# Kernel tuning notes

Hardware: AMD Instinct MI355X
Metric: run time of the kernel (lower is better)

Reference implementation:

```python
import jax, jax.numpy as jnp
import numpy as np

B, C, H, W = 2, 128, 96, 96
HEADS, DHEAD, WIN = 4, 32, 5
INNER = HEADS * DHEAD
PAD = WIN // 2


def setup_inputs() -> dict:
    key = jax.random.key(0)
    k1, k2, k3, k4, k5 = jax.random.split(key, 5)
    s = 1.0 / np.sqrt(C)
    return {
        "x": jax.random.normal(k1, (B, C, H, W), dtype=jnp.float32),
        "wq": jax.random.normal(k2, (INNER, C), dtype=jnp.float32) * s,
        "wk": jax.random.normal(k3, (INNER, C), dtype=jnp.float32) * s,
        "wv": jax.random.normal(k4, (INNER, C), dtype=jnp.float32) * s,
        "wproj": jax.random.normal(k5, (C, INNER), dtype=jnp.float32) * s,
    }


def _windows(t):
    # same neighborhood ordering as F.unfold (row-major over kernel offsets).
    tp = jnp.pad(t, ((0, 0), (0, 0), (0, 0), (PAD, PAD), (PAD, PAD)))
    wins = [tp[:, :, :, di:di + H, dj:dj + W]
            for di in range(WIN) for dj in range(WIN)]
    return jnp.stack(wins, axis=3)


def reference(x, wq, wk, wv, wproj):
    # 1x1 convs == per-pixel linear maps
    q = jnp.einsum('oc,bcxy->boxy', wq, x).reshape(B, HEADS, DHEAD, H, W)
    k = jnp.einsum('oc,bcxy->boxy', wk, x).reshape(B, HEADS, DHEAD, H, W)
    v = jnp.einsum('oc,bcxy->boxy', wv, x).reshape(B, HEADS, DHEAD, H, W)

    k_win = _windows(k)  # (B,h,d,25,H,W)
    v_win = _windows(v)

    scale = 1.0 / np.sqrt(DHEAD)
    attn = jnp.einsum('bhdxy,bhdkxy->bhkxy', q, k_win) * scale
    attn = jax.nn.softmax(attn, axis=2)  # softmax over the 25 window positions
    out = jnp.einsum('bhkxy,bhdkxy->bhdxy', attn, v_win)

    out = out.reshape(B, INNER, H, W)
    return jnp.einsum('co,boxy->bcxy', wproj, out)
```

## Files before the change

kernel.cpp:

```cpp
#include <hip/hip_runtime.h>
#include <hip/hip_fp16.h>

#define PP 9216

typedef _Float16 f16x8 __attribute__((ext_vector_type(8)));
typedef _Float16 f16x4 __attribute__((ext_vector_type(4)));
typedef _Float16 h2    __attribute__((ext_vector_type(2)));
typedef float    f32x4 __attribute__((ext_vector_type(4)));

#define LDS_BYTES 32768

__device__ __forceinline__ int swz128(int row, int hc) {
    return row * 128 + (((hc >> 3) ^ (row & 15)) << 3) + (hc & 7);
}
__device__ __forceinline__ int swz64(int row, int hc) {
    return row * 64 + (((hc >> 3) ^ (row & 7)) << 3) + (hc & 7);
}

__global__ __launch_bounds__(256) void prep_w(
    const float* __restrict__ wq, const float* __restrict__ wk,
    const float* __restrict__ wv, const float* __restrict__ wp,
    _Float16* __restrict__ wqkv16, _Float16* __restrict__ wp16)
{
    int e = (blockIdx.x * 256 + threadIdx.x) * 4;
    const float* src;
    _Float16* dst;
    if (e < 49152) {
        int o = e >> 7;
        src = (o < 128) ? (wq + (size_t)o * 128)
            : (o < 256) ? (wk + (size_t)(o - 128) * 128)
                        : (wv + (size_t)(o - 256) * 128);
        src += (e & 127);
        dst = wqkv16 + e;
    } else {
        int j = e - 49152;
        src = wp + j;
        dst = wp16 + j;
    }
    float4 v = *(const float4*)src;
    f16x4 h;
    h[0] = (_Float16)v.x; h[1] = (_Float16)v.y;
    h[2] = (_Float16)v.z; h[3] = (_Float16)v.w;
    *(f16x4*)dst = h;
}

__global__ __launch_bounds__(256, 5) void fused_attn(
    const float* __restrict__ x, const _Float16* __restrict__ wqkv,
    const _Float16* __restrict__ wp16, float* __restrict__ out)
{
    __shared__ __align__(16) char smem[LDS_BYTES];
    _Float16* sA = (_Float16*)smem;
    _Float16* sB = (_Float16*)(smem + 16384);

    const int t = threadIdx.x;
    const int w = t >> 6, lane = t & 63, lm = lane & 15, quad = lane >> 4;

    const int wgid = (blockIdx.x & 7) * 144 + (blockIdx.x >> 3);
    const int b = wgid / 576;
    const int rem = wgid - b * 576;
    const int x0 = (rem % 24) * 4, y0 = (rem / 24) * 4;

    const float* xb = x + (size_t)b * 128 * PP;
    float* ob = out + (size_t)b * 128 * PP;

    {
        const int pos = (t & 31) * 2;
        const int gy = y0 - 2 + (pos >> 3);
        const int gx = x0 - 2 + (pos & 7);
        const bool inb = ((unsigned)gy < 96u) && ((unsigned)gx < 96u);
        const float* src = xb + (size_t)(t >> 5) * PP + gy * 96 + gx;
        float2 vv[16];
        #pragma unroll
        for (int i = 0; i < 16; i++)
            vv[i] = inb ? *(const float2*)(src + (size_t)(i * 8) * PP)
                        : make_float2(0.f, 0.f);
        #pragma unroll
        for (int i = 0; i < 16; i++) {
            int c = i * 8 + (t >> 5);
            sA[swz128(pos,     c)] = (_Float16)vv[i].x;
            sA[swz128(pos + 1, c)] = (_Float16)vv[i].y;
        }
    }
    __syncthreads();

    h2 vpk[2][4][2];
    #pragma unroll
    for (int m = 0; m < 4; m++) {
        f16x8 A[4];
        #pragma unroll
        for (int kc = 0; kc < 4; kc++)
            A[kc] = *(const f16x8*)(sA + swz128(m * 16 + lm, kc * 32 + quad * 8));
        #pragma unroll
        for (int ni = 0; ni < 4; ni++) {
            const int wrow = (ni < 2) ? (128 + (w + 4 * ni) * 16 + lm)
                                      : (256 + (2 * w + (ni - 2)) * 16 + lm);
            const _Float16* wr = wqkv + (size_t)wrow * 128;
            f32x4 acc = {0.f, 0.f, 0.f, 0.f};
            #pragma unroll
            for (int kc = 0; kc < 4; kc++)
                acc = __builtin_amdgcn_mfma_f32_16x16x32_f16(
                    A[kc], *(const f16x8*)(wr + kc * 32 + quad * 8), acc, 0, 0, 0);
            if (ni < 2) {
                int n = w + 4 * ni;
                #pragma unroll
                for (int r = 0; r < 4; r++)
                    sB[swz128(m * 16 + quad * 4 + r, n * 16 + lm)] = (_Float16)acc[r];
            } else {
                h2 p0, p1;
                p0[0] = (_Float16)acc[0]; p0[1] = (_Float16)acc[1];
                p1[0] = (_Float16)acc[2]; p1[1] = (_Float16)acc[3];
                vpk[ni - 2][m][0] = p0;
                vpk[ni - 2][m][1] = p1;
            }
        }
    }

    f16x8 A3[4];
    {
        int hrow = ((lm >> 2) + 2) * 8 + (lm & 3) + 2;
        #pragma unroll
        for (int kc = 0; kc < 4; kc++)
            A3[kc] = *(const f16x8*)(sA + swz128(hrow, kc * 32 + quad * 8));
    }
    __syncthreads();

    _Float16* sQ = sA + 4608;
    #pragma unroll
    for (int nn = 0; nn < 2; nn++) {
        const _Float16* wr = wqkv + (size_t)((2 * w + nn) * 16 + lm) * 128;
        f32x4 acc = {0.f, 0.f, 0.f, 0.f};
        #pragma unroll
        for (int kc = 0; kc < 4; kc++)
            acc = __builtin_amdgcn_mfma_f32_16x16x32_f16(
                A3[kc], *(const f16x8*)(wr + kc * 32 + quad * 8), acc, 0, 0, 0);
        #pragma unroll
        for (int r = 0; r < 4; r++)
            sQ[swz128(quad * 4 + r, (2 * w + nn) * 16 + lm)] = (_Float16)acc[r];
    }

    f32x4 S[4];
    {
        f16x8 Aq = *(const f16x8*)(sQ + swz128(lm, w * 32 + quad * 8));
        #pragma unroll
        for (int n = 0; n < 4; n++) {
            f16x8 Bk = *(const f16x8*)(sB + swz128(n * 16 + lm, w * 32 + quad * 8));
            f32x4 z = {0.f, 0.f, 0.f, 0.f};
            S[n] = __builtin_amdgcn_mfma_f32_16x16x32_f16(Aq, Bk, z, 0, 0, 0);
        }
    }

    _Float16* sPh = sA + w * 1152;
    float inv4[4];
    {
        const float scale = 0.17677669529663689f;
        #pragma unroll
        for (int r = 0; r < 4; r++) {
            float e[4];
            float mx = -1e30f;
            #pragma unroll
            for (int n = 0; n < 4; n++) {
                int hy = n * 2 + (lm >> 3), hx = lm & 7;
                bool memb = (hy >= quad) && (hy < quad + 5) && (hx >= r) && (hx < r + 5);
                e[n] = memb ? S[n][r] * scale : -1e30f;
                mx = fmaxf(mx, e[n]);
            }
            mx = fmaxf(mx, __shfl_xor(mx, 1));
            mx = fmaxf(mx, __shfl_xor(mx, 2));
            mx = fmaxf(mx, __shfl_xor(mx, 4));
            mx = fmaxf(mx, __shfl_xor(mx, 8));
            float sum = 0.f;
            #pragma unroll
            for (int n = 0; n < 4; n++) {
                float ev = __expf(e[n] - mx);
                e[n] = ev;
                sum += ev;
            }
            sum += __shfl_xor(sum, 1);
            sum += __shfl_xor(sum, 2);
            sum += __shfl_xor(sum, 4);
            sum += __shfl_xor(sum, 8);
            inv4[r] = 1.f / sum;
            #pragma unroll
            for (int n = 0; n < 4; n++)
                sPh[(quad * 4 + r) * 72 + n * 16 + lm] = (_Float16)e[n];
        }
    }
    __syncthreads();

    _Float16* sVh = sB + w * 2048;
    #pragma unroll
    for (int nn = 0; nn < 2; nn++)
        #pragma unroll
        for (int m = 0; m < 4; m++)
            #pragma unroll
            for (int rp = 0; rp < 2; rp++)
                *(h2*)(sVh + swz64(nn * 16 + lm, m * 16 + quad * 4 + rp * 2))
                    = vpk[nn][m][rp];

    _Float16* sAo = sQ;
    {
        f16x8 Ap[2];
        #pragma unroll
        for (int kc = 0; kc < 2; kc++)
            Ap[kc] = *(const f16x8*)(sPh + lm * 72 + kc * 32 + quad * 8);
        #pragma unroll
        for (int nd = 0; nd < 2; nd++) {
            f32x4 acc = {0.f, 0.f, 0.f, 0.f};
            #pragma unroll
            for (int kc = 0; kc < 2; kc++) {
                f16x8 Bv = *(const f16x8*)(sVh + swz64(nd * 16 + lm, kc * 32 + quad * 8));
                acc = __builtin_amdgcn_mfma_f32_16x16x32_f16(Ap[kc], Bv, acc, 0, 0, 0);
            }
            #pragma unroll
            for (int r = 0; r < 4; r++)
                sAo[swz128(quad * 4 + r, w * 32 + nd * 16 + lm)] =
                    (_Float16)(acc[r] * inv4[r]);
        }
    }
    __syncthreads();

    {
        f16x8 Bf[4];
        #pragma unroll
        for (int kc = 0; kc < 4; kc++)
            Bf[kc] = *(const f16x8*)(sAo + swz128(lm, kc * 32 + quad * 8));
        int gp = (y0 + (lm >> 2)) * 96 + x0 + (lm & 3);
        #pragma unroll
        for (int mi = 0; mi < 2; mi++) {
            const _Float16* wr = wp16 + (size_t)((w * 2 + mi) * 16 + lm) * 128;
            f32x4 acc = {0.f, 0.f, 0.f, 0.f};
            #pragma unroll
            for (int kc = 0; kc < 4; kc++)
                acc = __builtin_amdgcn_mfma_f32_16x16x32_f16(
                    *(const f16x8*)(wr + kc * 32 + quad * 8), Bf[kc], acc, 0, 0, 0);
            int c0 = (w * 2 + mi) * 16 + quad * 4;
            #pragma unroll
            for (int r = 0; r < 4; r++)
                ob[(size_t)(c0 + r) * PP + gp] = acc[r];
        }
    }
}

extern "C" void kernel_launch(void* const* d_in, const int* in_sizes, int n_in,
                              void* d_out, int out_size, void* d_ws, size_t ws_size,
                              hipStream_t stream)
{
    const float* x  = (const float*)d_in[0];
    const float* wq = (const float*)d_in[1];
    const float* wk = (const float*)d_in[2];
    const float* wv = (const float*)d_in[3];
    const float* wp = (const float*)d_in[4];
    float* out = (float*)d_out;

    _Float16* wqkv16 = (_Float16*)d_ws;
    _Float16* wp16   = wqkv16 + 49152;

    prep_w<<<dim3(64), 256, 0, stream>>>(wq, wk, wv, wp, wqkv16, wp16);
    fused_attn<<<dim3(1152), 256, 0, stream>>>(x, wqkv16, wp16, out);
}
```

Before: 125.8 us.

## Split QKV projection into separate GEMM kernel to avoid halo recompute

Replaces the single fused kernel with two kernels. A standalone GEMM computes Q, K and V once per pixel into an fp16 pixel-major workspace. The attention kernel then gathers Q, K and V for each 4x4 tile plus its halo directly from global memory. This removes the roughly fourfold redundant K/V projection over 8x8 halo regions in the fused version, at the cost of an extra launch and a round trip of about 14 MB of fp16 intermediates through global memory and cache.

```diff
diff --git a/kernel.cpp b/kernel.cpp
--- a/kernel.cpp
+++ b/kernel.cpp
@@ -5,16 +5,20 @@
 
 typedef _Float16 f16x8 __attribute__((ext_vector_type(8)));
 typedef _Float16 f16x4 __attribute__((ext_vector_type(4)));
-typedef _Float16 h2    __attribute__((ext_vector_type(2)));
 typedef float    f32x4 __attribute__((ext_vector_type(4)));
-
-#define LDS_BYTES 32768
 
 __device__ __forceinline__ int swz128(int row, int hc) {
     return row * 128 + (((hc >> 3) ^ (row & 15)) << 3) + (hc & 7);
 }
 __device__ __forceinline__ int swz64(int row, int hc) {
     return row * 64 + (((hc >> 3) ^ (row & 7)) << 3) + (hc & 7);
+}
+
+__device__ __forceinline__ f16x8 zero8() {
+    f16x8 z;
+    #pragma unroll
+    for (int e = 0; e < 8; e++) z[e] = (_Float16)0;
+    return z;
 }
 
 __global__ __launch_bounds__(256) void prep_w(
@@ -44,14 +48,80 @@
     *(f16x4*)dst = h;
 }
 
-__global__ __launch_bounds__(256, 5) void fused_attn(
+__global__ __launch_bounds__(256) void qkv_gemm(
     const float* __restrict__ x, const _Float16* __restrict__ wqkv,
-    const _Float16* __restrict__ wp16, float* __restrict__ out)
-{
-    __shared__ __align__(16) char smem[LDS_BYTES];
-    _Float16* sA = (_Float16*)smem;
-    _Float16* sB = (_Float16*)(smem + 16384);
-
+    _Float16* __restrict__ qkvout)
+{
+    __shared__ __align__(16) char smem[43008];
+    _Float16* sX   = (_Float16*)smem;
+    _Float16* sEpi = (_Float16*)(smem + 16384);
+
+    const int t = threadIdx.x;
+    const int w = t >> 6, lane = t & 63, lm = lane & 15, quad = lane >> 4;
+    const int b = blockIdx.z;
+    const int p0 = blockIdx.x * 64;
+    const int nbase = blockIdx.y * 192;
+
+    const float* xb = x + (size_t)b * 128 * PP;
+    _Float16* qout = qkvout + (size_t)b * PP * 384;
+
+    {
+        const int px = t & 63;
+        const int c0 = (t >> 6) * 32;
+        #pragma unroll
+        for (int i = 0; i < 32; i++) {
+            float v = xb[(size_t)(c0 + i) * PP + p0 + px];
+            sX[swz128(px, c0 + i)] = (_Float16)v;
+        }
+    }
+    __syncthreads();
+
+    const int ms0 = (w & 1) * 32;
+    const int nw = (w >> 1) * 96;
+
+    f16x8 A[2][4];
+    #pragma unroll
+    for (int ms = 0; ms < 2; ms++)
+        #pragma unroll
+        for (int kc = 0; kc < 4; kc++)
+            A[ms][kc] = *(const f16x8*)(sX + swz128(ms0 + ms * 16 + lm, kc * 32 + quad * 8));
+
+    _Float16* strip = sEpi + w * 3328;
+    #pragma unroll
+    for (int nt = 0; nt < 6; nt++) {
+        const int o = nbase + nw + nt * 16 + lm;
+        const _Float16* wr = wqkv + (size_t)o * 128;
+        f16x8 Bf[4];
+        #pragma unroll
+        for (int kc = 0; kc < 4; kc++)
+            Bf[kc] = *(const f16x8*)(wr + kc * 32 + quad * 8);
+        #pragma unroll
+        for (int ms = 0; ms < 2; ms++) {
+            f32x4 acc = {0.f, 0.f, 0.f, 0.f};
+            #pragma unroll
+            for (int kc = 0; kc < 4; kc++)
+                acc = __builtin_amdgcn_mfma_f32_16x16x32_f16(A[ms][kc], Bf[kc], acc, 0, 0, 0);
+            #pragma unroll
+            for (int r = 0; r < 4; r++)
+                strip[(ms * 16 + quad * 4 + r) * 104 + nt * 16 + lm] = (_Float16)acc[r];
+        }
+    }
+
+    #pragma unroll
+    for (int it = 0; it < 6; it++) {
+        int idx = it * 64 + lane;
+        int row = idx / 12;
+        int ch  = idx % 12;
+        uint4 v = *(const uint4*)&strip[row * 104 + ch * 8];
+        *(uint4*)(qout + (size_t)(p0 + ms0 + row) * 384 + nbase + nw + ch * 8) = v;
+    }
+}
+
+__global__ __launch_bounds__(256, 4) void attn_fused(
+    const _Float16* __restrict__ qkv, const _Float16* __restrict__ wp16,
+    float* __restrict__ out)
+{
+    __shared__ __align__(16) char smem[28672];
     const int t = threadIdx.x;
     const int w = t >> 6, lane = t & 63, lm = lane & 15, quad = lane >> 4;
 
@@ -60,96 +130,50 @@
     const int rem = wgid - b * 576;
     const int x0 = (rem % 24) * 4, y0 = (rem / 24) * 4;
 
-    const float* xb = x + (size_t)b * 128 * PP;
+    const _Float16* qb = qkv + (size_t)b * PP * 384;
     float* ob = out + (size_t)b * 128 * PP;
 
-    {
-        const int pos = (t & 31) * 2;
-        const int gy = y0 - 2 + (pos >> 3);
-        const int gx = x0 - 2 + (pos & 7);
-        const bool inb = ((unsigned)gy < 96u) && ((unsigned)gx < 96u);
-        const float* src = xb + (size_t)(t >> 5) * PP + gy * 96 + gx;
-        float2 vv[16];
-        #pragma unroll
-        for (int i = 0; i < 16; i++)
-            vv[i] = inb ? *(const float2*)(src + (size_t)(i * 8) * PP)
-                        : make_float2(0.f, 0.f);
-        #pragma unroll
-        for (int i = 0; i < 16; i++) {
-            int c = i * 8 + (t >> 5);
-            sA[swz128(pos,     c)] = (_Float16)vv[i].x;
-            sA[swz128(pos + 1, c)] = (_Float16)vv[i].y;
-        }
-    }
-    __syncthreads();
-
-    h2 vpk[2][4][2];
-    #pragma unroll
-    for (int m = 0; m < 4; m++) {
-        f16x8 A[4];
-        #pragma unroll
-        for (int kc = 0; kc < 4; kc++)
-            A[kc] = *(const f16x8*)(sA + swz128(m * 16 + lm, kc * 32 + quad * 8));
-        #pragma unroll
-        for (int ni = 0; ni < 4; ni++) {
-            const int wrow = (ni < 2) ? (128 + (w + 4 * ni) * 16 + lm)
-                                      : (256 + (2 * w + (ni - 2)) * 16 + lm);
-            const _Float16* wr = wqkv + (size_t)wrow * 128;
-            f32x4 acc = {0.f, 0.f, 0.f, 0.f};
-            #pragma unroll
-            for (int kc = 0; kc < 4; kc++)
-                acc = __builtin_amdgcn_mfma_f32_16x16x32_f16(
-                    A[kc], *(const f16x8*)(wr + kc * 32 + quad * 8), acc, 0, 0, 0);
-            if (ni < 2) {
-                int n = w + 4 * ni;
-                #pragma unroll
-                for (int r = 0; r < 4; r++)
-                    sB[swz128(m * 16 + quad * 4 + r, n * 16 + lm)] = (_Float16)acc[r];
-            } else {
-                h2 p0, p1;
-                p0[0] = (_Float16)acc[0]; p0[1] = (_Float16)acc[1];
-                p1[0] = (_Float16)acc[2]; p1[1] = (_Float16)acc[3];
-                vpk[ni - 2][m][0] = p0;
-                vpk[ni - 2][m][1] = p1;
-            }
-        }
-    }
-
-    f16x8 A3[4];
-    {
-        int hrow = ((lm >> 2) + 2) * 8 + (lm & 3) + 2;
-        #pragma unroll
-        for (int kc = 0; kc < 4; kc++)
-            A3[kc] = *(const f16x8*)(sA + swz128(hrow, kc * 32 + quad * 8));
-    }
-    __syncthreads();
-
-    _Float16* sQ = sA + 4608;
-    #pragma unroll
-    for (int nn = 0; nn < 2; nn++) {
-        const _Float16* wr = wqkv + (size_t)((2 * w + nn) * 16 + lm) * 128;
-        f32x4 acc = {0.f, 0.f, 0.f, 0.f};
-        #pragma unroll
-        for (int kc = 0; kc < 4; kc++)
-            acc = __builtin_amdgcn_mfma_f32_16x16x32_f16(
-                A3[kc], *(const f16x8*)(wr + kc * 32 + quad * 8), acc, 0, 0, 0);
-        #pragma unroll
-        for (int r = 0; r < 4; r++)
-            sQ[swz128(quad * 4 + r, (2 * w + nn) * 16 + lm)] = (_Float16)acc[r];
-    }
+    _Float16* sVT = (_Float16*)(smem + w * 6144);
+    _Float16* sPh = (_Float16*)(smem + w * 6144 + 4096);
+    _Float16* sAo = (_Float16*)(smem + 24576);
+
+    {
+        const int pos = lane;
+        const int gy = y0 - 2 + (pos >> 3), gx = x0 - 2 + (pos & 7);
+        const bool valid = ((unsigned)gy < 96u) && ((unsigned)gx < 96u);
+        const int gp = valid ? (gy * 96 + gx) : 0;
+        const _Float16* vsrc = qb + (size_t)gp * 384 + 256 + w * 32;
+        f16x8 vv[4];
+        #pragma unroll
+        for (int j = 0; j < 4; j++) {
+            f16x8 ld = *(const f16x8*)(vsrc + j * 8);
+            vv[j] = valid ? ld : zero8();
+        }
+        #pragma unroll
+        for (int j = 0; j < 4; j++)
+            #pragma unroll
+            for (int e = 0; e < 8; e++) {
+                int d = j * 8 + e;
+                sVT[d * 64 + ((((pos >> 3)) ^ (d & 7)) << 3) + (pos & 7)] = vv[j][e];
+            }
+    }
+
+    const int gpq = (y0 + (lm >> 2)) * 96 + x0 + (lm & 3);
+    f16x8 Aq = *(const f16x8*)(qb + (size_t)gpq * 384 + w * 32 + quad * 8);
 
     f32x4 S[4];
-    {
-        f16x8 Aq = *(const f16x8*)(sQ + swz128(lm, w * 32 + quad * 8));
-        #pragma unroll
-        for (int n = 0; n < 4; n++) {
-            f16x8 Bk = *(const f16x8*)(sB + swz128(n * 16 + lm, w * 32 + quad * 8));
-            f32x4 z = {0.f, 0.f, 0.f, 0.f};
-            S[n] = __builtin_amdgcn_mfma_f32_16x16x32_f16(Aq, Bk, z, 0, 0, 0);
-        }
-    }
-
-    _Float16* sPh = sA + w * 1152;
+    #pragma unroll
+    for (int n = 0; n < 4; n++) {
+        int pos = n * 16 + lm;
+        int gy = y0 - 2 + (pos >> 3), gx = x0 - 2 + (pos & 7);
+        bool valid = ((unsigned)gy < 96u) && ((unsigned)gx < 96u);
+        int gp = valid ? (gy * 96 + gx) : 0;
+        f16x8 ld = *(const f16x8*)(qb + (size_t)gp * 384 + 128 + w * 32 + quad * 8);
+        f16x8 Bk = valid ? ld : zero8();
+        f32x4 z = {0.f, 0.f, 0.f, 0.f};
+        S[n] = __builtin_amdgcn_mfma_f32_16x16x32_f16(Aq, Bk, z, 0, 0, 0);
+    }
+
     float inv4[4];
     {
         const float scale = 0.17677669529663689f;
@@ -182,40 +206,30 @@
             inv4[r] = 1.f / sum;
             #pragma unroll
             for (int n = 0; n < 4; n++)
-                sPh[(quad * 4 + r) * 72 + n * 16 + lm] = (_Float16)e[n];
-        }
-    }
-    __syncthreads();
-
-    _Float16* sVh = sB + w * 2048;
-    #pragma unroll
-    for (int nn = 0; nn < 2; nn++)
-        #pragma unroll
-        for (int m = 0; m < 4; m++)
-            #pragma unroll
-            for (int rp = 0; rp < 2; rp++)
-                *(h2*)(sVh + swz64(nn * 16 + lm, m * 16 + quad * 4 + rp * 2))
-                    = vpk[nn][m][rp];
-
-    _Float16* sAo = sQ;
-    {
-        f16x8 Ap[2];
-        #pragma unroll
-        for (int kc = 0; kc < 2; kc++)
-            Ap[kc] = *(const f16x8*)(sPh + lm * 72 + kc * 32 + quad * 8);
-        #pragma unroll
-        for (int nd = 0; nd < 2; nd++) {
-            f32x4 acc = {0.f, 0.f, 0.f, 0.f};
-            #pragma unroll
-            for (int kc = 0; kc < 2; kc++) {
-                f16x8 Bv = *(const f16x8*)(sVh + swz64(nd * 16 + lm, kc * 32 + quad * 8));
-                acc = __builtin_amdgcn_mfma_f32_16x16x32_f16(Ap[kc], Bv, acc, 0, 0, 0);
-            }
+                sPh[swz64(quad * 4 + r, n * 16 + lm)] = (_Float16)e[n];
+        }
+    }
+
+    {
+        f32x4 acc2[2] = {{0.f, 0.f, 0.f, 0.f}, {0.f, 0.f, 0.f, 0.f}};
+        #pragma unroll
+        for (int kc = 0; kc < 2; kc++) {
+            f16x8 Ap = *(const f16x8*)(sPh + swz64(lm, kc * 32 + quad * 8));
+            #pragma unroll
+            for (int nd = 0; nd < 2; nd++) {
+                int row = nd * 16 + lm;
+                int hc = kc * 32 + quad * 8;
+                f16x8 Bv = *(const f16x8*)(sVT + row * 64
+                               + (((hc >> 3) ^ (row & 7)) << 3) + (hc & 7));
+                acc2[nd] = __builtin_amdgcn_mfma_f32_16x16x32_f16(Ap, Bv, acc2[nd], 0, 0, 0);
+            }
+        }
+        #pragma unroll
+        for (int nd = 0; nd < 2; nd++)
             #pragma unroll
             for (int r = 0; r < 4; r++)
                 sAo[swz128(quad * 4 + r, w * 32 + nd * 16 + lm)] =
-                    (_Float16)(acc[r] * inv4[r]);
-        }
+                    (_Float16)(acc2[nd][r] * inv4[r]);
     }
     __syncthreads();
 
@@ -254,7 +268,9 @@
 
     _Float16* wqkv16 = (_Float16*)d_ws;
     _Float16* wp16   = wqkv16 + 49152;
+    _Float16* qkvh   = wp16 + 16384;
 
     prep_w<<<dim3(64), 256, 0, stream>>>(wq, wk, wv, wp, wqkv16, wp16);
-    fused_attn<<<dim3(1152), 256, 0, stream>>>(x, wqkv16, wp16, out);
-}
+    qkv_gemm<<<dim3(144, 2, 2), 256, 0, stream>>>(x, wqkv16, qkvh);
+    attn_fused<<<dim3(1152), 256, 0, stream>>>(qkvh, wp16, out);
+}
```

Result: faster. 103.4 us (-17.8%).
